# Kernel optimization log

Hardware: AMD Instinct MI355X
Metric: run time of the kernel (lower is better)

The kernel has to match this reference:

```python
import jax, jax.numpy as jnp
import numpy as np

N = 3072
F_IN = 512
H1 = 256
HFC = 64
OUT_DIM = 16
NUM_POOL = 3
P_CUT = 30.0  # ps[0]: percentile threshold on positive attention entries
CC_ITERS = 16  # min-label propagation w/ pointer jumping; reach >= 2^16 hops


def l2norm(x):
    # torch F.normalize(p=2, dim=1)
    return x / jnp.clip(jnp.linalg.norm(x, axis=1, keepdims=True), 1e-12, None)


def gcn(x, adj, W, b):
    # standard Kipf GraphConvolution: adj @ (x @ W) + b
    return adj @ (x @ W) + b


def normalize_adj(adj, k):
    n = adj.shape[0]
    A = adj + k * jnp.eye(n, dtype=adj.dtype)
    D = jnp.sqrt(A.sum(0))
    return A / (D[:, None] * D[None, :])


def edge_score(x, adj, a, W, b):
    h = x @ W + b                               # (n, HFC)
    s1 = h @ a[:HFC]                            # (n,)
    s2 = h @ a[HFC:]
    e = jax.nn.sigmoid(s1[:, None] + s2[None, :])
    att = jnp.where(adj > 0, e, jnp.zeros((), e.dtype))
    att = 0.5 * (att + att.T)
    i = jnp.arange(att.shape[0])
    return att.at[i, i].set(1.0)


def percentile_pos(att, p):
    # np.percentile(att[att>0], p) with linear interpolation, jit-safe
    pos = att > 0
    n_pos = pos.sum()
    s = jnp.sort(jnp.where(pos, att, jnp.inf).ravel())
    idx = (n_pos - 1).astype(att.dtype) * (p / 100.0)
    lo = jnp.floor(idx).astype(jnp.int32)
    hi = jnp.ceil(idx).astype(jnp.int32)
    frac = idx - lo.astype(att.dtype)
    return s[lo] * (1.0 - frac) + s[hi] * frac


def cc_labels(mask):
    # connected components via min-label propagation + pointer jumping.
    # diag of mask is always True (att diag = 1), so every node has a neighbor.
    n = mask.shape[0]
    def step(labels, _):
        neigh = jnp.min(jnp.where(mask, labels[None, :], n), axis=1)
        new = jnp.minimum(labels, neigh)
        new = new[new]  # pointer jumping doubles reach each iter
        return new, None
    labels, _ = jax.lax.scan(step, jnp.arange(n, dtype=jnp.int32), None, length=CC_ITERS)
    return labels


def pool(x, adj, att, p):
    cut = percentile_pos(att, p)
    att = att * (att >= cut).astype(att.dtype)
    labels = jax.lax.stop_gradient(cc_labels(att > 0))
    # fixed-shape membership: cluster id = representative (min) node index, padded to N
    C = jax.nn.one_hot(labels, att.shape[0], dtype=x.dtype).T  # (n_clusters=n, n)
    a2 = C @ adj @ C.T
    a2 = 0.5 * (a2 + a2.T)
    cnt = (att > 0).sum(1).astype(x.dtype)  # >=1 since diag survives the cut
    x2 = C @ ((att / cnt[:, None]) @ x)
    return x2, a2, C


def forward(x, adjC, adj, encW0, encb0, encW, encb, fcW, fcb, aW, decW, decb, decW_out, decb_out):
    adjs = [adj]
    adjCs = [adjC]
    xs, Cs, atts = [], [], []
    # ----- encode -----
    for k in range(NUM_POOL):
        x1 = x
        W, b = (encW0, encb0) if k == 0 else (encW[k - 1], encb[k - 1])
        h = jax.nn.relu(gcn(x, adjCs[-1], W, b))
        x = l2norm(h) if k == 0 else l2norm(h + x1)  # residual added for layer idx > 0
        xs.append(x)
        att = edge_score(x, adjs[-1], aW[k], fcW[k], fcb[k])
        x, adjk, C = pool(x, adjs[-1], att, P_CUT)
        adjCk = normalize_adj(adjk, 1.0)  # pool's adjC output is discarded in the original
        x = l2norm(x)
        adjs.append(adjk)
        adjCs.append(adjCk)
        atts.append(att)
        Cs.append(C)
    x = l2norm(jax.nn.elu(gcn(x, adjCs[-1], encW[NUM_POOL - 1], encb[NUM_POOL - 1])))
    xs.append(x)
    # ----- decode -----
    for k in range(NUM_POOL):
        lev = NUM_POOL - k - 1
        x = Cs[lev].T @ x                       # unpool; C is already binary
        x = jnp.concatenate([x, xs[lev]], axis=1)
        x = l2norm(jax.nn.elu(gcn(x, adjCs[lev], decW[k], decb[k])))
    x = gcn(x, adjCs[0], decW_out, decb_out)
    logp = jax.nn.log_softmax(x, axis=1)
    return logp, jnp.stack(Cs), jnp.stack(atts)


def setup_inputs() -> dict:
    key = jax.random.key(0)
    ks = jax.random.split(key, 12)
    x = jax.random.normal(ks[0], (N, F_IN), jnp.float32)
    u = jax.random.uniform(ks[1], (N, N))
    m = (u < 16.0 / N).astype(jnp.float32)  # avg degree ~16
    adj = jnp.maximum(m, m.T)
    i = jnp.arange(N)
    adj = adj.at[i, i].set(1.0)
    adjC = normalize_adj(adj, 1.0)

    def xav(k, shape):
        fan_in = shape[-2] if len(shape) > 1 else shape[-1]
        return jax.random.normal(k, shape, jnp.float32) * (1.0 / np.sqrt(fan_in))

    return {
        "x": x, "adjC": adjC, "adj": adj,
        "encW0": xav(ks[2], (F_IN, H1)), "encb0": jnp.zeros((H1,), jnp.float32),
        "encW": xav(ks[3], (NUM_POOL, H1, H1)), "encb": jnp.zeros((NUM_POOL, H1), jnp.float32),
        "fcW": xav(ks[4], (NUM_POOL, H1, HFC)), "fcb": jnp.zeros((NUM_POOL, HFC), jnp.float32),
        "aW": xav(ks[5], (NUM_POOL, 2 * HFC)),
        "decW": xav(ks[6], (NUM_POOL, 2 * H1, H1)), "decb": jnp.zeros((NUM_POOL, H1), jnp.float32),
        "decW_out": xav(ks[7], (H1, OUT_DIM)), "decb_out": jnp.zeros((OUT_DIM,), jnp.float32),
    }


def reference(x, adjC, adj, encW0, encb0, encW, encb, fcW, fcb, aW, decW, decb, decW_out, decb_out):
    return forward(x, adjC, adj, encW0, encb0, encW, encb, fcW, fcb, aW, decW, decb, decW_out, decb_out)
```

## Files before the change

kernel.cpp:

```cpp
#include <hip/hip_runtime.h>
#include <math.h>

#define NN 3072
#define FF 256
#define CAPE (1<<18)
#define MAXCH 3200

struct Scal {
  int nnzS, nnz2, nzero, mtot, ncht;
  int lo, hi, rank_rem, below_acc, c_le;
  unsigned prefix, vlo, minabove;
  float frac, cut;
};

__device__ __forceinline__ float sigm(float x){ return 1.0f/(1.0f+expf(-x)); }

__global__ __launch_bounds__(256) void k_count_dense(const float* __restrict__ A, int* __restrict__ rowcnt, float* __restrict__ Drow){
  int i=blockIdx.x, t=threadIdx.x;
  int c=0; float sm=0.f;
  for(int j=t;j<NN;j+=256){ float a=A[(size_t)i*NN+j]; if(a!=0.0f||j==i) c++; sm+=a; }
  __shared__ int s[256]; __shared__ float fs[256];
  s[t]=c; fs[t]=sm; __syncthreads();
  for(int o=128;o;o>>=1){ if(t<o){ s[t]+=s[t+o]; fs[t]+=fs[t+o]; } __syncthreads(); }
  if(t==0){ rowcnt[i]=s[0]; if(Drow) Drow[i]=sqrtf(fs[0]+1.0f); }
}

__global__ __launch_bounds__(1024) void k_scan(const int* __restrict__ cnt, int* __restrict__ rp, int* __restrict__ total){
  int t=threadIdx.x;
  int a0=cnt[t*3+0], a1=cnt[t*3+1], a2=cnt[t*3+2];
  int loc=a0+a1+a2;
  __shared__ int s[1024];
  s[t]=loc; __syncthreads();
  for(int o=1;o<1024;o<<=1){ int v=(t>=o)?s[t-o]:0; __syncthreads(); s[t]+=v; __syncthreads(); }
  int excl=s[t]-loc;
  rp[t*3+0]=excl; rp[t*3+1]=excl+a0; rp[t*3+2]=excl+a0+a1;
  if(t==1023){ rp[NN]=s[t]; *total=s[t]; }
}

__global__ __launch_bounds__(256) void k_fill_dense(const float* __restrict__ A, const float* __restrict__ ACd, const float* __restrict__ D,
    const int* __restrict__ rp, int* __restrict__ rows, int* __restrict__ cols, float* __restrict__ aval, float* __restrict__ acval){
  int i=blockIdx.x, t=threadIdx.x;
  const int CH=NN/256;
  int j0=t*CH; int c=0;
  for(int u=0;u<CH;u++){ int j=j0+u; float a=A[(size_t)i*NN+j]; if(a!=0.0f||j==i) c++; }
  __shared__ int s[256]; s[t]=c; __syncthreads();
  for(int o=1;o<256;o<<=1){ int v=(t>=o)?s[t-o]:0; __syncthreads(); s[t]+=v; __syncthreads(); }
  int pos=rp[i]+s[t]-c;
  float Di = D?D[i]:0.0f;
  for(int u=0;u<CH;u++){ int j=j0+u; float a=A[(size_t)i*NN+j];
    if(a!=0.0f||j==i){
      if(pos<CAPE){
        rows[pos]=i; cols[pos]=j; aval[pos]=a;
        acval[pos]= ACd? ACd[(size_t)i*NN+j] : (a+(j==i?1.0f:0.0f))/(Di*D[j]);
      }
      pos++;
    }
  }
}

__global__ __launch_bounds__(256) void k_gemm(const float* __restrict__ A, const float* __restrict__ B, float* __restrict__ C,
                                              int M, int K, int Nc){
  __shared__ float As[16][68];
  __shared__ float Bs[16][68];
  int tid=threadIdx.x;
  int tx=tid&15, ty=tid>>4;
  int bm=blockIdx.y*64, bn=blockIdx.x*64;
  int lm=tid>>2, lk=(tid&3)*4;
  int kr=tid>>4, nf=(tid&15)*4;
  float acc[4][4]={};
  for(int k0=0;k0<K;k0+=16){
    float4 a4=*(const float4*)(A+(size_t)(bm+lm)*K+k0+lk);
    As[lk+0][lm]=a4.x; As[lk+1][lm]=a4.y; As[lk+2][lm]=a4.z; As[lk+3][lm]=a4.w;
    float4 b4=*(const float4*)(B+(size_t)(k0+kr)*Nc+bn+nf);
    *(float4*)&Bs[kr][nf]=b4;
    __syncthreads();
#pragma unroll
    for(int kk=0;kk<16;kk++){
      float4 av=*(const float4*)&As[kk][ty*4];
      float4 bv=*(const float4*)&Bs[kk][tx*4];
      float am[4]={av.x,av.y,av.z,av.w};
      float bb[4]={bv.x,bv.y,bv.z,bv.w};
#pragma unroll
      for(int i2=0;i2<4;i2++)
#pragma unroll
        for(int j2=0;j2<4;j2++) acc[i2][j2]+=am[i2]*bb[j2];
    }
    __syncthreads();
  }
  for(int i2=0;i2<4;i2++){
    float4 o=make_float4(acc[i2][0],acc[i2][1],acc[i2][2],acc[i2][3]);
    *(float4*)(C+(size_t)(bm+ty*4+i2)*Nc+bn+tx*4)=o;
  }
}

__global__ __launch_bounds__(256) void k_gemm16(const float* __restrict__ X, const float* __restrict__ W, float* __restrict__ T){
  int idx=blockIdx.x*256+threadIdx.x;
  if(idx>=NN*16) return;
  int i=idx>>4, o=idx&15;
  float s=0.f;
  for(int kk=0;kk<FF;kk++) s+=X[(size_t)i*FF+kk]*W[kk*16+o];
  T[idx]=s;
}

__global__ __launch_bounds__(256) void k_spmm_gcn(const int* __restrict__ rp, const int* __restrict__ cols, const float* __restrict__ vals,
    const float* __restrict__ X, const float* __restrict__ bias, const float* __restrict__ resid, float* __restrict__ out, int act){
  int wid=blockIdx.x*4+(threadIdx.x>>6);
  int lane=threadIdx.x&63;
  if(wid>=NN) return;
  int e0=rp[wid], e1=rp[wid+1];
  float4 acc=make_float4(0,0,0,0);
  for(int e=e0;e<e1;e++){
    float v=vals[e]; int c=cols[e];
    float4 xv=*(const float4*)(X+(size_t)c*FF+lane*4);
    acc.x+=v*xv.x; acc.y+=v*xv.y; acc.z+=v*xv.z; acc.w+=v*xv.w;
  }
  float4 bv=*(const float4*)(bias+lane*4);
  acc.x+=bv.x; acc.y+=bv.y; acc.z+=bv.z; acc.w+=bv.w;
  if(act==0){
    acc.x=fmaxf(acc.x,0.f); acc.y=fmaxf(acc.y,0.f); acc.z=fmaxf(acc.z,0.f); acc.w=fmaxf(acc.w,0.f);
  } else {
    acc.x=acc.x>0.f?acc.x:expm1f(acc.x); acc.y=acc.y>0.f?acc.y:expm1f(acc.y);
    acc.z=acc.z>0.f?acc.z:expm1f(acc.z); acc.w=acc.w>0.f?acc.w:expm1f(acc.w);
  }
  if(resid){
    float4 r=*(const float4*)(resid+(size_t)wid*FF+lane*4);
    acc.x+=r.x; acc.y+=r.y; acc.z+=r.z; acc.w+=r.w;
  }
  float ss=acc.x*acc.x+acc.y*acc.y+acc.z*acc.z+acc.w*acc.w;
  for(int o=32;o;o>>=1) ss+=__shfl_xor(ss,o);
  float nrm=fmaxf(sqrtf(ss),1e-12f);
  float4 o4=make_float4(acc.x/nrm,acc.y/nrm,acc.z/nrm,acc.w/nrm);
  *(float4*)(out+(size_t)wid*FF+lane*4)=o4;
}

__global__ __launch_bounds__(256) void k_spmm_plain(const int* __restrict__ rp, const int* __restrict__ cols, const float* __restrict__ vals,
    const float* __restrict__ X, float* __restrict__ out){
  int wid=blockIdx.x*4+(threadIdx.x>>6);
  int lane=threadIdx.x&63;
  if(wid>=NN) return;
  int e0=rp[wid], e1=rp[wid+1];
  float4 acc=make_float4(0,0,0,0);
  for(int e=e0;e<e1;e++){
    if(e>=CAPE) break;
    float v=vals[e]; int c=cols[e];
    float4 xv=*(const float4*)(X+(size_t)c*FF+lane*4);
    acc.x+=v*xv.x; acc.y+=v*xv.y; acc.z+=v*xv.z; acc.w+=v*xv.w;
  }
  *(float4*)(out+(size_t)wid*FF+lane*4)=acc;
}

__global__ __launch_bounds__(64) void k_edge(const float* __restrict__ X, const float* __restrict__ fw, const float* __restrict__ fb,
    const float* __restrict__ av, float* __restrict__ s1, float* __restrict__ s2, Scal* sc){
  int i=blockIdx.x, l=threadIdx.x;
  if(i==0&&l==0) sc->nzero=0;
  __shared__ float xr[FF];
  *(float4*)&xr[l*4]=*(const float4*)(X+(size_t)i*FF+l*4);
  __syncthreads();
  float h=fb[l];
  for(int kk=0;kk<FF;kk++) h+=xr[kk]*fw[kk*64+l];
  float p1=h*av[l], p2=h*av[64+l];
  for(int o=32;o;o>>=1){ p1+=__shfl_xor(p1,o); p2+=__shfl_xor(p2,o); }
  if(l==0){ s1[i]=p1; s2[i]=p2; }
}

__global__ __launch_bounds__(256) void k_att_row(const int* __restrict__ rp, const int* __restrict__ cols,
    const float* __restrict__ s1, const float* __restrict__ s2, float* __restrict__ attD, float* __restrict__ cand, Scal* sc){
  __shared__ float row[NN];
  __shared__ int wred[4];
  int i=blockIdx.x, t=threadIdx.x;
  for(int j=t;j<NN;j+=256) row[j]=0.f;
  __syncthreads();
  int e0=rp[i], e1=rp[i+1];
  float s1i=s1[i], s2i=s2[i];
  int nz=0;
  for(int e=e0+t;e<e1;e+=256){
    int j=cols[e];
    float v=(j==i)?1.0f:0.5f*(sigm(s1i+s2[j])+sigm(s1[j]+s2i));
    row[j]=v;
    if(e<CAPE) cand[e]=v;
    if(!(v>0.f)) nz++;
  }
  for(int o=32;o;o>>=1) nz+=__shfl_xor(nz,o);
  if((t&63)==0) wred[t>>6]=nz;
  __syncthreads();
  if(t==0){ int s=wred[0]+wred[1]+wred[2]+wred[3]; if(s) atomicAdd(&sc->nzero,s); }
  float* orow=attD+(size_t)i*NN;
  for(int j=t*4;j<NN;j+=1024) *(float4*)(orow+j)=*(const float4*)&row[j];
}

template<int PHASE>
__global__ __launch_bounds__(256) void k_hist(const float* __restrict__ cand, const Scal* __restrict__ sc, unsigned* __restrict__ bins){
  const int NB = (PHASE==0)?16384:256;
  __shared__ unsigned h[NB];
  int t=threadIdx.x;
  for(int b=t;b<NB;b+=256) h[b]=0;
  __syncthreads();
  int n=sc->nnzS; if(n>CAPE) n=CAPE;
  unsigned pref=sc->prefix;
  int stride=gridDim.x*256;
  for(int e=blockIdx.x*256+t; e<n; e+=stride){
    float v=cand[e];
    if(!(v>0.f)) continue;
    unsigned bb=__float_as_uint(v);
    if(PHASE==0) atomicAdd(&h[bb>>16],1u);
    else if(PHASE==1){ if((bb>>16)==pref) atomicAdd(&h[(bb>>8)&0xFFu],1u); }
    else { if((bb>>8)==pref) atomicAdd(&h[bb&0xFFu],1u); }
  }
  __syncthreads();
  for(int b=t;b<NB;b+=256){ unsigned c=h[b]; if(c) atomicAdd(&bins[b],c); }
}

template<int PHASE>
__global__ __launch_bounds__(256) void k_pick(unsigned* __restrict__ bins, Scal* sc){
  const int NB=(PHASE==0)?16384:256;
  const int PER=NB/256;
  __shared__ int part[256];
  __shared__ int selbin; __shared__ int below_sel; __shared__ int sh_r;
  int t=threadIdx.x;
  if(t==0){
    int r;
    if(PHASE==0){
      int np=sc->nnzS - sc->nzero;
      float idx=(float)(np-1)*(30.0f/100.0f);
      float fl=floorf(idx), ce=ceilf(idx);
      sc->lo=(int)fl; sc->hi=(int)ce; sc->frac=idx-fl;
      sc->below_acc=0; sc->minabove=0xFFFFFFFFu;
      r=(int)fl;
    } else r=sc->rank_rem;
    sh_r=r;
  }
  __syncthreads();
  int r=sh_r;
  int b0=t*PER;
  int sum=0;
  for(int u=0;u<PER;u++) sum+=(int)bins[b0+u];
  part[t]=sum; __syncthreads();
  for(int o=1;o<256;o<<=1){ int v=(t>=o)?part[t-o]:0; __syncthreads(); part[t]+=v; __syncthreads(); }
  int incl=part[t], excl=incl-sum;
  if(r>=excl && r<incl){
    int run=excl;
    for(int u=0;u<PER;u++){
      int c=(int)bins[b0+u];
      if(r<run+c){ selbin=b0+u; below_sel=run; break; }
      run+=c;
    }
  }
  __syncthreads();
  if(t==0){
    sc->rank_rem=r-below_sel;
    sc->below_acc+=below_sel;
    if(PHASE==0) sc->prefix=(unsigned)selbin;
    else if(PHASE==1) sc->prefix=(sc->prefix<<8)|(unsigned)selbin;
    else{
      sc->vlo=(sc->prefix<<8)|(unsigned)selbin;
      sc->c_le=sc->below_acc+(int)bins[selbin];
    }
  }
  if(PHASE<2){
    __syncthreads();
    if(t<256) bins[t]=0;
  }
}

__global__ __launch_bounds__(256) void k_minabove(const float* __restrict__ cand, Scal* sc){
  int n=sc->nnzS; if(n>CAPE) n=CAPE;
  unsigned vlo=sc->vlo;
  int tid=threadIdx.x, lane=tid&63;
  int stride=gridDim.x*256;
  for(int base=blockIdx.x*256; base<n; base+=stride){
    int e=base+tid;
    unsigned b=0xFFFFFFFFu;
    if(e<n){ float v=cand[e]; if(v>0.f){ unsigned bb=__float_as_uint(v); if(bb>vlo) b=bb; } }
    for(int o=32;o;o>>=1){ unsigned ob=__shfl_xor(b,o); b=ob<b?ob:b; }
    if(lane==0&&b!=0xFFFFFFFFu) atomicMin(&sc->minabove,b);
  }
}

__global__ void k_cut(Scal* sc){
  float slo=__uint_as_float(sc->vlo);
  float shi;
  if(sc->hi==sc->lo) shi=slo;
  else if(sc->c_le>sc->hi) shi=slo;
  else shi=__uint_as_float(sc->minabove);
  sc->cut=slo*(1.0f-sc->frac)+shi*sc->frac;
}

__global__ __launch_bounds__(256) void k_pc_count(const int* __restrict__ rp, const float* __restrict__ cand, const Scal* __restrict__ sc,
    int* __restrict__ rowcnt, float* __restrict__ cntf){
  int wid=blockIdx.x*4+(threadIdx.x>>6);
  int lane=threadIdx.x&63;
  if(wid>=NN) return;
  int e0=rp[wid], e1=rp[wid+1];
  float cut=sc->cut;
  int c=0;
  for(int e=e0+lane;e<e1;e+=64){ if(e<CAPE && cand[e]>=cut) c++; }
  for(int o=32;o;o>>=1) c+=__shfl_xor(c,o);
  if(lane==0){ rowcnt[wid]=c; cntf[wid]=(float)c; }
}

__global__ __launch_bounds__(256) void k_pc_fill(const int* __restrict__ rp, const int* __restrict__ cols, const float* __restrict__ cand,
    const Scal* __restrict__ sc, const int* __restrict__ rp2, int* __restrict__ rows2, int* __restrict__ cols2, float* __restrict__ pval,
    const float* __restrict__ cntf){
  int wid=blockIdx.x*4+(threadIdx.x>>6);
  int lane=threadIdx.x&63;
  if(wid>=NN) return;
  int e0=rp[wid], e1=rp[wid+1];
  float cut=sc->cut, cf=cntf[wid];
  int base=rp2[wid];
  for(int eb=e0;eb<e1;eb+=64){
    int e=eb+lane;
    bool p=(e<e1)&&(e<CAPE)&&(cand[e]>=cut);
    unsigned long long m=__ballot(p);
    if(p){
      int pos=base+__popcll(m&((1ull<<lane)-1ull));
      if(pos<CAPE){ rows2[pos]=wid; cols2[pos]=cols[e]; pval[pos]=cand[e]/cf; }
    }
    base+=__popcll(m);
  }
}

__global__ __launch_bounds__(1024) void k_cc(const int* __restrict__ rows2, const int* __restrict__ cols2, Scal* sc,
    int* __restrict__ labk, int* __restrict__ moff_g, int* __restrict__ memb,
    int* __restrict__ choff_g, int* __restrict__ chm0_g, int* __restrict__ chm1_g){
  __shared__ int lab[NN];
  __shared__ int cnt[NN];
  __shared__ int mof[NN];
  __shared__ int s[1024];
  __shared__ int chg;
  int t=threadIdx.x;
  for(int i=t;i<NN;i+=1024){ lab[i]=i; cnt[i]=0; }
  int n2=sc->nnz2; if(n2>CAPE) n2=CAPE;
  __syncthreads();
  for(int it=0;it<16;it++){
    if(t==0) chg=0;
    __syncthreads();
    for(int e=t;e<n2;e+=1024){
      int i=rows2[e], j=cols2[e];
      if(i<j){
        int li=lab[i], lj=lab[j];
        if(lj<li){ if(atomicMin(&lab[i],lj)>lj) chg=1; }
        else if(li<lj){ if(atomicMin(&lab[j],li)>li) chg=1; }
      }
    }
    __syncthreads();
    int l0=lab[t], l1=lab[t+1024], l2=lab[t+2048];
    int v0=lab[l0], v1=lab[l1], v2=lab[l2];
    __syncthreads();
    if(v0<l0){ lab[t]=v0; chg=1; }
    if(v1<l1){ lab[t+1024]=v1; chg=1; }
    if(v2<l2){ lab[t+2048]=v2; chg=1; }
    __syncthreads();
    if(!chg) break;
    __syncthreads();
  }
  for(int i=t;i<NN;i+=1024){ int l=lab[i]; labk[i]=l; atomicAdd(&cnt[l],1); }
  __syncthreads();
  int a0=cnt[t*3+0], a1=cnt[t*3+1], a2=cnt[t*3+2];
  int loc=a0+a1+a2;
  s[t]=loc; __syncthreads();
  for(int o=1;o<1024;o<<=1){ int v=(t>=o)?s[t-o]:0; __syncthreads(); s[t]+=v; __syncthreads(); }
  int excl=s[t]-loc;
  __syncthreads();
  mof[t*3+0]=excl; mof[t*3+1]=excl+a0; mof[t*3+2]=excl+a0+a1;
  cnt[t*3+0]=excl; cnt[t*3+1]=excl+a0; cnt[t*3+2]=excl+a0+a1;
  moff_g[t*3+0]=excl; moff_g[t*3+1]=excl+a0; moff_g[t*3+2]=excl+a0+a1;
  if(t==1023) moff_g[NN]=s[t];
  __syncthreads();
  int ch0=(a0+63)>>6, ch1=(a1+63)>>6, ch2=(a2+63)>>6;
  int locc=ch0+ch1+ch2;
  s[t]=locc; __syncthreads();
  for(int o=1;o<1024;o<<=1){ int v=(t>=o)?s[t-o]:0; __syncthreads(); s[t]+=v; __syncthreads(); }
  int cexcl=s[t]-locc;
  choff_g[t*3+0]=cexcl; choff_g[t*3+1]=cexcl+ch0; choff_g[t*3+2]=cexcl+ch0+ch1;
  if(t==1023){ choff_g[NN]=s[t]; sc->ncht=s[t]; }
  {
    int bases[3]={cexcl,cexcl+ch0,cexcl+ch0+ch1};
    int cnts[3]={a0,a1,a2};
    int nqs[3]={ch0,ch1,ch2};
    for(int u=0;u<3;u++){
      int m0=mof[t*3+u];
      int me=m0+cnts[u];
      for(int q=0;q<nqs[u];q++){
        int idx=bases[u]+q;
        if(idx<MAXCH){
          chm0_g[idx]=m0+q*64;
          int e2=m0+q*64+64; chm1_g[idx]=e2<me?e2:me;
        }
      }
    }
  }
  __syncthreads();
  int lane=t&63, wv=t>>6;
  for(int b=0;b<3;b++){
    int j=b*1024+t;
    int myl=lab[j];
    int rank_w=0,total=0;
#pragma unroll
    for(int l=0;l<64;l++){
      int lb=__shfl(myl,l);
      if(lb==myl){ total++; if(l<lane) rank_w++; }
    }
    for(int w=0;w<16;w++){
      if(wv==w){
        int base=cnt[myl];
        memb[base+rank_w]=j;
        if(rank_w==0) cnt[myl]=base+total;
      }
      __syncthreads();
    }
  }
}

__global__ __launch_bounds__(256) void k_a2e(const int* __restrict__ rowsA, const int* __restrict__ colsA_, const float* __restrict__ aval,
    const Scal* __restrict__ sc, const int* __restrict__ labk, float* __restrict__ dense){
  int e=blockIdx.x*256+threadIdx.x;
  int n=sc->nnzS; if(n>CAPE) n=CAPE;
  int lane=threadIdx.x&63;
  bool valid=(e<n);
  float a=valid?aval[e]:0.f;
  valid=valid&&(a!=0.f);
  int key=0;
  if(valid) key=labk[rowsA[e]]*NN+labk[colsA_[e]];
  unsigned long long act=__ballot(valid);
  while(act){
    int leader=__ffsll(act)-1;
    int lkey=__shfl(key,leader);
    bool same=valid&&(key==lkey);
    float contrib=same?a:0.f;
    for(int o=32;o;o>>=1) contrib+=__shfl_xor(contrib,o);
    if(lane==leader) atomicAdd(&dense[(size_t)lkey],contrib);
    act&=~__ballot(same);
  }
}

__global__ __launch_bounds__(256) void k_x2p(const float* __restrict__ y, const int* __restrict__ memb,
    const int* __restrict__ chm0, const int* __restrict__ chm1, const Scal* __restrict__ sc, float* __restrict__ partial){
  int b=blockIdx.x;
  if(b>=sc->ncht||b>=MAXCH) return;
  int t=threadIdx.x;
  int m0=chm0[b], m1=chm1[b];
  float acc=0.f;
#pragma unroll 4
  for(int m=m0;m<m1;m++) acc+=y[(size_t)memb[m]*FF+t];
  partial[(size_t)b*FF+t]=acc;
}
__global__ __launch_bounds__(256) void k_x2f(const int* __restrict__ choff, const float* __restrict__ partial, float* __restrict__ out){
  int c=blockIdx.x, t=threadIdx.x;
  int q0=choff[c], q1=choff[c+1];
  float acc=0.f;
  for(int q=q0;q<q1&&q<MAXCH;q++) acc+=partial[(size_t)q*FF+t];
  __shared__ float red[256];
  red[t]=acc*acc; __syncthreads();
  for(int o=128;o;o>>=1){ if(t<o) red[t]+=red[t+o]; __syncthreads(); }
  float nrm=fmaxf(sqrtf(red[0]),1e-12f);
  out[(size_t)c*FF+t]=(q1>q0)?acc/nrm:0.f;
}

__global__ __launch_bounds__(256) void k_gather(const float* __restrict__ X, const int* __restrict__ labs, const float* __restrict__ xsk,
    float* __restrict__ xcat){
  int idx=blockIdx.x*256+threadIdx.x;
  if(idx>=NN*128) return;
  int j=idx>>7, f4=idx&127;
  float4 v;
  if(f4<64) v=*(const float4*)(X+(size_t)labs[j]*FF+f4*4);
  else v=*(const float4*)(xsk+(size_t)j*FF+(size_t)(f4-64)*4);
  *(float4*)(xcat+(size_t)j*512+(size_t)f4*4)=v;
}

__global__ __launch_bounds__(256) void k_final(const int* __restrict__ rp, const int* __restrict__ cols, const float* __restrict__ vals,
    const float* __restrict__ T, const float* __restrict__ bias, float* __restrict__ logp){
  int i=blockIdx.x*256+threadIdx.x;
  if(i>=NN) return;
  float o[16];
#pragma unroll
  for(int f=0;f<16;f++) o[f]=bias[f];
  int e1=rp[i+1];
  for(int e=rp[i];e<e1;e++){
    float v=vals[e]; const float* tr=T+(size_t)cols[e]*16;
#pragma unroll
    for(int f=0;f<16;f++) o[f]+=v*tr[f];
  }
  float m=o[0];
#pragma unroll
  for(int f=1;f<16;f++) m=fmaxf(m,o[f]);
  float ssum=0.f;
#pragma unroll
  for(int f=0;f<16;f++) ssum+=expf(o[f]-m);
  float lse=logf(ssum);
#pragma unroll
  for(int f=0;f<16;f++) logp[(size_t)i*16+f]=o[f]-m-lse;
}

__global__ __launch_bounds__(256) void k_cs_full(const int* __restrict__ labsv, float* __restrict__ CsB){
  int idx=blockIdx.x*256+threadIdx.x;
  const int ROW4=NN/4;
  int l=idx/(NN*ROW4);
  int rem=idx-l*(NN*ROW4);
  int c=rem/ROW4;
  int j4=(rem-c*ROW4)*4;
  const int* lb=labsv+(size_t)l*NN+j4;
  int4 lv=*(const int4*)lb;
  float4 o;
  o.x=(lv.x==c)?1.0f:0.0f;
  o.y=(lv.y==c)?1.0f:0.0f;
  o.z=(lv.z==c)?1.0f:0.0f;
  o.w=(lv.w==c)?1.0f:0.0f;
  *(float4*)(CsB+(size_t)idx*4)=o;
}

extern "C" void kernel_launch(void* const* d_in, const int* in_sizes, int n_in,
                              void* d_out, int out_size, void* d_ws, size_t ws_size,
                              hipStream_t stream) {
  (void)in_sizes; (void)n_in; (void)out_size;
  const float* x_in =(const float*)d_in[0];
  const float* adjC =(const float*)d_in[1];
  const float* adj  =(const float*)d_in[2];
  const float* encW0=(const float*)d_in[3];
  const float* encb0=(const float*)d_in[4];
  const float* encW =(const float*)d_in[5];
  const float* encb =(const float*)d_in[6];
  const float* fcW  =(const float*)d_in[7];
  const float* fcb  =(const float*)d_in[8];
  const float* aW   =(const float*)d_in[9];
  const float* decW =(const float*)d_in[10];
  const float* decb =(const float*)d_in[11];
  const float* decWo=(const float*)d_in[12];
  const float* decbo=(const float*)d_in[13];
  float* out=(float*)d_out;

  float* logp=out;
  float* CsB = out + (size_t)NN*16;
  float* attB= CsB + 3ull*NN*NN;
  float* slot1 = CsB + (size_t)NN*NN;
  float* xs[4]; for(int i=0;i<4;i++) xs[i]=slot1+(size_t)i*NN*FF;
  float* xcur=slot1+(size_t)4*NN*FF;
  float* ybuf=slot1+(size_t)5*NN*FF;
  float* tbuf=slot1+(size_t)6*NN*FF;
  float* slot2 = CsB + 2ull*NN*NN;
  float* xcat=slot2;
  float* t16 = xcat + (size_t)NN*512;

  char* w=(char*)d_ws; size_t off=0;
  auto alc=[&](size_t b)->void*{ off=(off+255)&~(size_t)255; void* r=w+off; off+=b; return r; };
  Scal* sc=(Scal*)alc(sizeof(Scal));
  int* rowcnt=(int*)alc((size_t)NN*4);
  int* rp[4]; for(int i=0;i<4;i++) rp[i]=(int*)alc((size_t)(NN+1)*4);
  int* rp2=(int*)alc((size_t)(NN+1)*4);
  int* colsA[4]; float* acv[4];
  for(int i=0;i<4;i++){ colsA[i]=(int*)alc((size_t)CAPE*4); acv[i]=(float*)alc((size_t)CAPE*4); }
  float* avalS=(float*)alc((size_t)CAPE*4);
  int* rowsA=(int*)alc((size_t)CAPE*4);
  float* cand=(float*)alc((size_t)CAPE*4);
  int* rows2=(int*)alc((size_t)CAPE*4);
  int* cols2=(int*)alc((size_t)CAPE*4);
  float* pval=(float*)alc((size_t)CAPE*4);
  unsigned* bins=(unsigned*)alc((size_t)16384*4);
  int* labsv=(int*)alc((size_t)3*NN*4);
  int* moff=(int*)alc((size_t)(NN+1)*4);
  int* memb=(int*)alc((size_t)NN*4);
  int* choff=(int*)alc((size_t)(NN+1)*4);
  int* chm0=(int*)alc((size_t)MAXCH*4);
  int* chm1=(int*)alc((size_t)MAXCH*4);
  float* partial=(float*)alc((size_t)MAXCH*FF*4);
  float* cntf=(float*)alc((size_t)NN*4);
  float* s1=(float*)alc((size_t)NN*4);
  float* s2v=(float*)alc((size_t)NN*4);
  float* Dv=(float*)alc((size_t)NN*4);
  float* dense;
  size_t denseB=(size_t)NN*NN*4;
  if(ws_size>=off+denseB+4096) dense=(float*)alc(denseB);
  else dense=CsB;

  auto build_csr=[&](const float* Ad, const float* ACd, const float* Dp, int lvl){
    k_count_dense<<<NN,256,0,stream>>>(Ad,rowcnt,Dv);
    k_scan<<<1,1024,0,stream>>>(rowcnt,rp[lvl],&sc->nnzS);
    k_fill_dense<<<NN,256,0,stream>>>(Ad,ACd,Dp,rp[lvl],rowsA,colsA[lvl],avalS,acv[lvl]);
  };

  build_csr(adj,adjC,nullptr,0);

  for(int k=0;k<3;k++){
    const float* xin=(k==0)?x_in:xcur;
    const float* Wk=(k==0)?encW0:(encW+(size_t)(k-1)*FF*FF);
    const float* bk=(k==0)?encb0:(encb+(size_t)(k-1)*FF);
    int K=(k==0)?512:FF;
    k_gemm<<<dim3(FF/64,NN/64),256,0,stream>>>(xin,Wk,tbuf,NN,K,FF);
    k_spmm_gcn<<<NN/4,256,0,stream>>>(rp[k],colsA[k],acv[k],tbuf,bk,(k==0)?nullptr:xcur,xs[k],0);

    k_edge<<<NN,64,0,stream>>>(xs[k],fcW+(size_t)k*FF*64,fcb+(size_t)k*64,aW+(size_t)k*128,s1,s2v,sc);
    k_att_row<<<NN,256,0,stream>>>(rp[k],colsA[k],s1,s2v,attB+(size_t)k*NN*NN,cand,sc);

    hipMemsetAsync(bins,0,(size_t)16384*4,stream);
    k_hist<0><<<64,256,0,stream>>>(cand,sc,bins);
    k_pick<0><<<1,256,0,stream>>>(bins,sc);
    k_hist<1><<<64,256,0,stream>>>(cand,sc,bins);
    k_pick<1><<<1,256,0,stream>>>(bins,sc);
    k_hist<2><<<64,256,0,stream>>>(cand,sc,bins);
    k_pick<2><<<1,256,0,stream>>>(bins,sc);
    k_minabove<<<256,256,0,stream>>>(cand,sc);
    k_cut<<<1,1,0,stream>>>(sc);

    k_pc_count<<<NN/4,256,0,stream>>>(rp[k],cand,sc,rowcnt,cntf);
    k_scan<<<1,1024,0,stream>>>(rowcnt,rp2,&sc->nnz2);
    k_pc_fill<<<NN/4,256,0,stream>>>(rp[k],colsA[k],cand,sc,rp2,rows2,cols2,pval,cntf);

    k_cc<<<1,1024,0,stream>>>(rows2,cols2,sc,labsv+(size_t)k*NN,moff,memb,choff,chm0,chm1);

    hipMemsetAsync(dense,0,denseB,stream);
    k_a2e<<<CAPE/256,256,0,stream>>>(rowsA,colsA[k],avalS,sc,labsv+(size_t)k*NN,dense);

    k_spmm_plain<<<NN/4,256,0,stream>>>(rp2,cols2,pval,xs[k],ybuf);
    k_x2p<<<MAXCH,256,0,stream>>>(ybuf,memb,chm0,chm1,sc,partial);
    k_x2f<<<NN,256,0,stream>>>(choff,partial,xcur);

    build_csr(dense,nullptr,Dv,k+1);
  }

  k_gemm<<<dim3(FF/64,NN/64),256,0,stream>>>(xcur,encW+(size_t)2*FF*FF,tbuf,NN,FF,FF);
  k_spmm_gcn<<<NN/4,256,0,stream>>>(rp[3],colsA[3],acv[3],tbuf,encb+(size_t)2*FF,nullptr,xs[3],1);

  float* xd=xs[3];
  float* outsb[3]={xcur,ybuf,xcur};
  for(int k=0;k<3;k++){
    int lev=2-k;
    k_gather<<<(NN*128)/256,256,0,stream>>>(xd,labsv+(size_t)lev*NN,xs[lev],xcat);
    k_gemm<<<dim3(FF/64,NN/64),256,0,stream>>>(xcat,decW+(size_t)k*512*FF,tbuf,NN,512,FF);
    k_spmm_gcn<<<NN/4,256,0,stream>>>(rp[lev],colsA[lev],acv[lev],tbuf,decb+(size_t)k*FF,nullptr,outsb[k],1);
    xd=outsb[k];
  }

  k_gemm16<<<(NN*16)/256,256,0,stream>>>(xd,decWo,t16);
  k_final<<<(NN+255)/256,256,0,stream>>>(rp[0],colsA[0],acv[0],t16,decbo,logp);

  k_cs_full<<<(3*NN*(NN/4))/256,256,0,stream>>>(labsv,CsB);
}
```

Baseline: 912.1 us.

## Replace three-pass radix select with histogram, bucket compaction, and single-block refine

The percentile selection previously ran three histogram passes over all candidate attention values, plus a separate min-above pass and a cut kernel, and issued a memset each level. Now a single 16-bit-prefix histogram picks the bucket. One pass then compacts the elements in that bucket into a buffer and computes the minimum above the bucket. A single 1024-thread block finishes the low 16 bits and computes the cut. This cuts kernel launches and full passes over the candidate array. The trade-off is that the final refine runs in one block, which is slow if the selected bucket holds many elements.

```diff
diff --git a/kernel.cpp b/kernel.cpp
--- a/kernel.cpp
+++ b/kernel.cpp
@@ -7,13 +7,18 @@
 #define MAXCH 3200
 
 struct Scal {
-  int nnzS, nnz2, nzero, mtot, ncht;
-  int lo, hi, rank_rem, below_acc, c_le;
-  unsigned prefix, vlo, minabove;
+  int nnzS, nnz2, nzero, ncht, ccount;
+  int lo, hi, rank_rem, below_acc;
+  unsigned prefix, minabove;
   float frac, cut;
 };
 
 __device__ __forceinline__ float sigm(float x){ return 1.0f/(1.0f+expf(-x)); }
+
+__global__ __launch_bounds__(256) void k_init(unsigned* __restrict__ bins){
+  int i=blockIdx.x*256+threadIdx.x;
+  if(i<16384) bins[i]=0;
+}
 
 __global__ __launch_bounds__(256) void k_count_dense(const float* __restrict__ A, int* __restrict__ rowcnt, float* __restrict__ Drow){
   int i=blockIdx.x, t=threadIdx.x;
@@ -188,58 +193,44 @@
   for(int j=t*4;j<NN;j+=1024) *(float4*)(orow+j)=*(const float4*)&row[j];
 }
 
-template<int PHASE>
-__global__ __launch_bounds__(256) void k_hist(const float* __restrict__ cand, const Scal* __restrict__ sc, unsigned* __restrict__ bins){
-  const int NB = (PHASE==0)?16384:256;
-  __shared__ unsigned h[NB];
+__global__ __launch_bounds__(256) void k_hist14(const float* __restrict__ cand, const Scal* __restrict__ sc, unsigned* __restrict__ bins){
+  __shared__ unsigned h[16384];
   int t=threadIdx.x;
-  for(int b=t;b<NB;b+=256) h[b]=0;
+  for(int b=t;b<16384;b+=256) h[b]=0;
   __syncthreads();
   int n=sc->nnzS; if(n>CAPE) n=CAPE;
-  unsigned pref=sc->prefix;
   int stride=gridDim.x*256;
   for(int e=blockIdx.x*256+t; e<n; e+=stride){
     float v=cand[e];
-    if(!(v>0.f)) continue;
-    unsigned bb=__float_as_uint(v);
-    if(PHASE==0) atomicAdd(&h[bb>>16],1u);
-    else if(PHASE==1){ if((bb>>16)==pref) atomicAdd(&h[(bb>>8)&0xFFu],1u); }
-    else { if((bb>>8)==pref) atomicAdd(&h[bb&0xFFu],1u); }
-  }
-  __syncthreads();
-  for(int b=t;b<NB;b+=256){ unsigned c=h[b]; if(c) atomicAdd(&bins[b],c); }
-}
-
-template<int PHASE>
-__global__ __launch_bounds__(256) void k_pick(unsigned* __restrict__ bins, Scal* sc){
-  const int NB=(PHASE==0)?16384:256;
-  const int PER=NB/256;
+    if(v>0.f) atomicAdd(&h[__float_as_uint(v)>>16],1u);
+  }
+  __syncthreads();
+  for(int b=t;b<16384;b+=256){ unsigned c=h[b]; if(c) atomicAdd(&bins[b],c); }
+}
+
+__global__ __launch_bounds__(256) void k_pick14(unsigned* __restrict__ bins, Scal* sc){
   __shared__ int part[256];
   __shared__ int selbin; __shared__ int below_sel; __shared__ int sh_r;
   int t=threadIdx.x;
   if(t==0){
-    int r;
-    if(PHASE==0){
-      int np=sc->nnzS - sc->nzero;
-      float idx=(float)(np-1)*(30.0f/100.0f);
-      float fl=floorf(idx), ce=ceilf(idx);
-      sc->lo=(int)fl; sc->hi=(int)ce; sc->frac=idx-fl;
-      sc->below_acc=0; sc->minabove=0xFFFFFFFFu;
-      r=(int)fl;
-    } else r=sc->rank_rem;
-    sh_r=r;
+    int np=sc->nnzS - sc->nzero;
+    float idx=(float)(np-1)*(30.0f/100.0f);
+    float fl=floorf(idx), ce=ceilf(idx);
+    sc->lo=(int)fl; sc->hi=(int)ce; sc->frac=idx-fl;
+    sc->ccount=0; sc->minabove=0xFFFFFFFFu;
+    sh_r=(int)fl;
   }
   __syncthreads();
   int r=sh_r;
-  int b0=t*PER;
+  int b0=t*64;
   int sum=0;
-  for(int u=0;u<PER;u++) sum+=(int)bins[b0+u];
+  for(int u=0;u<64;u++) sum+=(int)bins[b0+u];
   part[t]=sum; __syncthreads();
   for(int o=1;o<256;o<<=1){ int v=(t>=o)?part[t-o]:0; __syncthreads(); part[t]+=v; __syncthreads(); }
   int incl=part[t], excl=incl-sum;
   if(r>=excl && r<incl){
     int run=excl;
-    for(int u=0;u<PER;u++){
+    for(int u=0;u<64;u++){
       int c=(int)bins[b0+u];
       if(r<run+c){ selbin=b0+u; below_sel=run; break; }
       run+=c;
@@ -248,41 +239,89 @@
   __syncthreads();
   if(t==0){
     sc->rank_rem=r-below_sel;
-    sc->below_acc+=below_sel;
-    if(PHASE==0) sc->prefix=(unsigned)selbin;
-    else if(PHASE==1) sc->prefix=(sc->prefix<<8)|(unsigned)selbin;
-    else{
-      sc->vlo=(sc->prefix<<8)|(unsigned)selbin;
-      sc->c_le=sc->below_acc+(int)bins[selbin];
-    }
-  }
-  if(PHASE<2){
-    __syncthreads();
-    if(t<256) bins[t]=0;
-  }
-}
-
-__global__ __launch_bounds__(256) void k_minabove(const float* __restrict__ cand, Scal* sc){
+    sc->below_acc=below_sel;
+    sc->prefix=(unsigned)selbin;
+  }
+  for(int b=t;b<16384;b+=256) bins[b]=0;
+}
+
+__global__ __launch_bounds__(256) void k_collect(const float* __restrict__ cand, Scal* sc, unsigned* __restrict__ collbuf){
   int n=sc->nnzS; if(n>CAPE) n=CAPE;
-  unsigned vlo=sc->vlo;
+  unsigned pref=sc->prefix;
   int tid=threadIdx.x, lane=tid&63;
   int stride=gridDim.x*256;
   for(int base=blockIdx.x*256; base<n; base+=stride){
     int e=base+tid;
-    unsigned b=0xFFFFFFFFu;
-    if(e<n){ float v=cand[e]; if(v>0.f){ unsigned bb=__float_as_uint(v); if(bb>vlo) b=bb; } }
-    for(int o=32;o;o>>=1){ unsigned ob=__shfl_xor(b,o); b=ob<b?ob:b; }
-    if(lane==0&&b!=0xFFFFFFFFu) atomicMin(&sc->minabove,b);
-  }
-}
-
-__global__ void k_cut(Scal* sc){
-  float slo=__uint_as_float(sc->vlo);
-  float shi;
-  if(sc->hi==sc->lo) shi=slo;
-  else if(sc->c_le>sc->hi) shi=slo;
-  else shi=__uint_as_float(sc->minabove);
-  sc->cut=slo*(1.0f-sc->frac)+shi*sc->frac;
+    unsigned bb=0; bool inb=false; unsigned above=0xFFFFFFFFu;
+    if(e<n){
+      float v=cand[e];
+      if(v>0.f){
+        bb=__float_as_uint(v);
+        unsigned key=bb>>16;
+        if(key==pref) inb=true;
+        else if(key>pref) above=bb;
+      }
+    }
+    unsigned long long bal=__ballot(inb);
+    if(bal){
+      int leader=__ffsll(bal)-1;
+      int cnt=__popcll(bal);
+      int wbase=0;
+      if(lane==leader) wbase=atomicAdd(&sc->ccount,cnt);
+      wbase=__shfl(wbase,leader);
+      if(inb){
+        int rk=__popcll(bal&((1ull<<lane)-1ull));
+        if(wbase+rk<CAPE) collbuf[wbase+rk]=bb;
+      }
+    }
+    for(int o=32;o;o>>=1){ unsigned ob=__shfl_xor(above,o); above=ob<above?ob:above; }
+    if(lane==0&&above!=0xFFFFFFFFu) atomicMin(&sc->minabove,above);
+  }
+}
+
+__global__ __launch_bounds__(1024) void k_sel2(const unsigned* __restrict__ collbuf, Scal* sc){
+  __shared__ unsigned h[256];
+  __shared__ int sel1, below1, sel2, below2, cnt2;
+  __shared__ unsigned red[1024];
+  int t=threadIdx.x;
+  int n=sc->ccount; if(n>CAPE) n=CAPE;
+  int r=sc->rank_rem;
+  if(t<256) h[t]=0;
+  __syncthreads();
+  for(int e=t;e<n;e+=1024) atomicAdd(&h[(collbuf[e]>>8)&0xFFu],1u);
+  __syncthreads();
+  if(t==0){
+    int run=0;
+    for(int b=0;b<256;b++){ int c=(int)h[b]; if(r<run+c){ sel1=b; below1=run; break; } run+=c; }
+  }
+  __syncthreads();
+  int s1b=sel1;
+  int r2=r-below1;
+  __syncthreads();
+  if(t<256) h[t]=0;
+  __syncthreads();
+  for(int e=t;e<n;e+=1024){ unsigned bb=collbuf[e]; if(((bb>>8)&0xFFu)==(unsigned)s1b) atomicAdd(&h[bb&0xFFu],1u); }
+  __syncthreads();
+  if(t==0){
+    int run=0;
+    for(int b=0;b<256;b++){ int c=(int)h[b]; if(r2<run+c){ sel2=b; below2=run; cnt2=c; break; } run+=c; }
+  }
+  __syncthreads();
+  unsigned vlo=(sc->prefix<<16)|((unsigned)s1b<<8)|(unsigned)sel2;
+  unsigned mn=0xFFFFFFFFu;
+  for(int e=t;e<n;e+=1024){ unsigned bb=collbuf[e]; if(bb>vlo&&bb<mn) mn=bb; }
+  red[t]=mn; __syncthreads();
+  for(int o=512;o;o>>=1){ if(t<o){ unsigned ob=red[t+o]; if(ob<red[t]) red[t]=ob; } __syncthreads(); }
+  if(t==0){
+    unsigned minab=red[0]<sc->minabove?red[0]:sc->minabove;
+    int c_le=sc->below_acc+below1+below2+cnt2;
+    float slo=__uint_as_float(vlo);
+    float shi;
+    if(sc->hi==sc->lo) shi=slo;
+    else if(c_le>sc->hi) shi=slo;
+    else shi=__uint_as_float(minab);
+    sc->cut=slo*(1.0f-sc->frac)+shi*sc->frac;
+  }
 }
 
 __global__ __launch_bounds__(256) void k_pc_count(const int* __restrict__ rp, const float* __restrict__ cand, const Scal* __restrict__ sc,
@@ -551,6 +590,7 @@
   float* avalS=(float*)alc((size_t)CAPE*4);
   int* rowsA=(int*)alc((size_t)CAPE*4);
   float* cand=(float*)alc((size_t)CAPE*4);
+  unsigned* collbuf=(unsigned*)alc((size_t)CAPE*4);
   int* rows2=(int*)alc((size_t)CAPE*4);
   int* cols2=(int*)alc((size_t)CAPE*4);
   float* pval=(float*)alc((size_t)CAPE*4);
@@ -577,6 +617,7 @@
     k_fill_dense<<<NN,256,0,stream>>>(Ad,ACd,Dp,rp[lvl],rowsA,colsA[lvl],avalS,acv[lvl]);
   };
 
+  k_init<<<64,256,0,stream>>>(bins);
   build_csr(adj,adjC,nullptr,0);
 
   for(int k=0;k<3;k++){
@@ -590,15 +631,10 @@
     k_edge<<<NN,64,0,stream>>>(xs[k],fcW+(size_t)k*FF*64,fcb+(size_t)k*64,aW+(size_t)k*128,s1,s2v,sc);
     k_att_row<<<NN,256,0,stream>>>(rp[k],colsA[k],s1,s2v,attB+(size_t)k*NN*NN,cand,sc);
 
-    hipMemsetAsync(bins,0,(size_t)16384*4,stream);
-    k_hist<0><<<64,256,0,stream>>>(cand,sc,bins);
-    k_pick<0><<<1,256,0,stream>>>(bins,sc);
-    k_hist<1><<<64,256,0,stream>>>(cand,sc,bins);
-    k_pick<1><<<1,256,0,stream>>>(bins,sc);
-    k_hist<2><<<64,256,0,stream>>>(cand,sc,bins);
-    k_pick<2><<<1,256,0,stream>>>(bins,sc);
-    k_minabove<<<256,256,0,stream>>>(cand,sc);
-    k_cut<<<1,1,0,stream>>>(sc);
+    k_hist14<<<64,256,0,stream>>>(cand,sc,bins);
+    k_pick14<<<1,256,0,stream>>>(bins,sc);
+    k_collect<<<64,256,0,stream>>>(cand,sc,collbuf);
+    k_sel2<<<1,1024,0,stream>>>(collbuf,sc);
 
     k_pc_count<<<NN/4,256,0,stream>>>(rp[k],cand,sc,rowcnt,cntf);
     k_scan<<<1,1024,0,stream>>>(rowcnt,rp2,&sc->nnz2);
```

Result: no change. 915.6 us (+0.4%).
